# Kernel optimization log

Hardware: AMD Instinct MI355X
Metric: run time of the kernel (lower is better)

## Reference

```python
import jax, jax.numpy as jnp
import numpy as np

VOCAB, D, MAX_LEN = 32000, 256, 128
BATCH, SEQ = 32, 128


def setup_inputs() -> dict:
    key = jax.random.key(0)
    ks = jax.random.split(key, 8)
    s = 1.0 / np.sqrt(D)  # torch nn.Linear default init scale
    X = jax.random.randint(ks[0], (BATCH, SEQ), 0, VOCAB)
    emb = jax.random.normal(ks[1], (VOCAB, D), dtype=jnp.float32)
    W_l = jax.random.uniform(ks[2], (D, D), minval=-s, maxval=s, dtype=jnp.float32)
    b_l = jax.random.uniform(ks[3], (D,), minval=-s, maxval=s, dtype=jnp.float32)
    W_r = jax.random.uniform(ks[4], (D, D), minval=-s, maxval=s, dtype=jnp.float32)
    b_r = jax.random.uniform(ks[5], (D,), minval=-s, maxval=s, dtype=jnp.float32)
    W_rn = jax.random.uniform(ks[6], (D, D), minval=-s, maxval=s, dtype=jnp.float32)
    b_rn = jax.random.uniform(ks[7], (D,), minval=-s, maxval=s, dtype=jnp.float32)
    return {"X": X, "emb": emb, "W_l": W_l, "b_l": b_l,
            "W_r": W_r, "b_r": b_r, "W_rn": W_rn, "b_rn": b_rn}


def reference(X, emb, W_l, b_l, W_r, b_r, W_rn, b_rn):
    X = X[:, :MAX_LEN]
    n = X.shape[1]
    Xe = emb[X]                               # (B, n, D) embedding lookup
    Xl = Xe @ W_l.T + b_l                     # (B, n, D)
    Xr = Xe @ W_r.T + b_r                     # (B, n, D)
    # pairwise: pair[b, i, j] = relu(Xl[b, j] + Xr[b, i])  -> (B, n, n, D)
    pair = jax.nn.relu(Xl[:, None, :, :] + Xr[:, :, None, :])
    # linear_rn then sum over (i, j); by linearity: sum(pair) @ W_rn.T + n^2 * b_rn
    pooled = pair.sum(axis=(1, 2))            # (B, D)
    return pooled @ W_rn.T + (n * n) * b_rn   # (B, D)
```

## Files before the change

kernel.cpp:

```cpp
#include <hip/hip_runtime.h>

#define D 256
#define S 128
#define B 32
#define RT 8
#define DC 16

__device__ __forceinline__ float dot4(float4 a, float4 b) {
    return a.x * b.x + a.y * b.y + a.z * b.z + a.w * b.w;
}

__global__ __launch_bounds__(256) void k1_gemm(
    const int* __restrict__ X, const float* __restrict__ emb,
    const float* __restrict__ Wl, const float* __restrict__ bl,
    const float* __restrict__ Wr, const float* __restrict__ br,
    float* __restrict__ Xl, float* __restrict__ Xr)
{
    __shared__ float4 As[RT][D / 4];

    const int tid = threadIdx.x;
    const int rowBase = blockIdx.x * RT;

    {
        const int f0 = tid;
        const int f1 = tid + 256;
        const int r0 = f0 >> 6, kf0 = f0 & 63;
        const int r1 = f1 >> 6, kf1 = f1 & 63;
        const int tok0 = X[rowBase + r0];
        const int tok1 = X[rowBase + r1];
        As[r0][kf0] = ((const float4*)(emb + (size_t)tok0 * D))[kf0];
        As[r1][kf1] = ((const float4*)(emb + (size_t)tok1 * D))[kf1];
    }
    __syncthreads();

    const int d = tid;
    const float4* __restrict__ wl4 = (const float4*)(Wl + (size_t)d * D);
    const float4* __restrict__ wr4 = (const float4*)(Wr + (size_t)d * D);

    float accl[RT], accr[RT];
#pragma unroll
    for (int r = 0; r < RT; ++r) { accl[r] = 0.f; accr[r] = 0.f; }

#pragma unroll 4
    for (int kk = 0; kk < D / 4; ++kk) {
        const float4 wlv = wl4[kk];
        const float4 wrv = wr4[kk];
#pragma unroll
        for (int r = 0; r < RT; ++r) {
            const float4 a = As[r][kk];
            accl[r] += dot4(a, wlv);
            accr[r] += dot4(a, wrv);
        }
    }
    const float bld = bl[d], brd = br[d];
#pragma unroll
    for (int r = 0; r < RT; ++r) {
        Xl[(size_t)(rowBase + r) * D + d] = accl[r] + bld;
        Xr[(size_t)(rowBase + r) * D + d] = accr[r] + brd;
    }
}

__global__ __launch_bounds__(256) void k2_pairsum(
    const float* __restrict__ Xl, const float* __restrict__ Xr,
    float* __restrict__ pooled)
{
    __shared__ float lxl[S * DC];
    __shared__ float lxr[S * DC];
    __shared__ float red[256];

    const int b   = blockIdx.x >> 4;
    const int dc  = blockIdx.x & 15;
    const int tid = threadIdx.x;
    const int dl  = tid & (DC - 1);
    const int ig  = tid >> 4;

    const size_t base = (size_t)b * S * D + (size_t)dc * DC;
    {
        float4* lxl4 = (float4*)lxl;
        float4* lxr4 = (float4*)lxr;
#pragma unroll
        for (int t = 0; t < 2; ++t) {
            const int e4 = tid + t * 256;
            const int j = e4 >> 2, df = e4 & 3;
            const float4* pl = (const float4*)(Xl + base + (size_t)j * D);
            const float4* pr = (const float4*)(Xr + base + (size_t)j * D);
            lxl4[e4] = pl[df];
            lxr4[e4] = pr[df];
        }
    }
    __syncthreads();

    float xr[8];
    float sr = 0.f;
#pragma unroll
    for (int u = 0; u < 8; ++u) {
        xr[u] = lxr[(ig * 8 + u) * DC + dl];
        sr += xr[u];
    }

    float sabs = 0.f, sxl = 0.f;
#pragma unroll 4
    for (int j = 0; j < S; ++j) {
        const float x = lxl[j * DC + dl];
        sxl += x;
#pragma unroll
        for (int u = 0; u < 8; ++u)
            sabs += fabsf(x + xr[u]);
    }

    red[tid] = sabs + (float)S * sr;
    __syncthreads();

    if (tid < DC) {
        float tot = 0.f;
#pragma unroll
        for (int g = 0; g < 16; ++g) tot += red[g * DC + tid];
        pooled[(size_t)b * D + (size_t)dc * DC + tid] =
            0.5f * ((float)S * sxl + tot);
    }
}

__global__ __launch_bounds__(256) void k3_out(
    const float* __restrict__ pooled, const float* __restrict__ Wrn,
    const float* __restrict__ brn, float* __restrict__ out)
{
    __shared__ float lp[D];
    __shared__ float red[256];
    const int bb = blockIdx.x >> 3;
    const int dc = blockIdx.x & 7;
    const int tid = threadIdx.x;
    lp[tid] = pooled[(size_t)bb * D + tid];
    __syncthreads();

    const int dl = tid & 31;
    const int kg = tid >> 5;
    const int d = dc * 32 + dl;
    const float4* __restrict__ w4 = (const float4*)(Wrn + (size_t)d * D) + kg * 8;
    const float4* __restrict__ p4 = (const float4*)lp + kg * 8;
    float acc = 0.f;
#pragma unroll
    for (int f = 0; f < 8; ++f) acc += dot4(w4[f], p4[f]);

    red[tid] = acc;
    __syncthreads();
    if (tid < 32) {
        float s = 0.f;
#pragma unroll
        for (int g = 0; g < 8; ++g) s += red[g * 32 + tid];
        out[(size_t)bb * D + dc * 32 + tid] = s + (float)(S * S) * brn[dc * 32 + tid];
    }
}

extern "C" void kernel_launch(void* const* d_in, const int* in_sizes, int n_in,
                              void* d_out, int out_size, void* d_ws, size_t ws_size,
                              hipStream_t stream) {
    const int*   X   = (const int*)d_in[0];
    const float* emb = (const float*)d_in[1];
    const float* Wl  = (const float*)d_in[2];
    const float* bl  = (const float*)d_in[3];
    const float* Wr  = (const float*)d_in[4];
    const float* br  = (const float*)d_in[5];
    const float* Wrn = (const float*)d_in[6];
    const float* brn = (const float*)d_in[7];
    float* out = (float*)d_out;

    float* ws     = (float*)d_ws;
    float* Xl     = ws;
    float* Xr     = ws + (size_t)B * S * D;
    float* pooled = ws + 2 * (size_t)B * S * D;

    k1_gemm<<<(B * S) / RT, 256, 0, stream>>>(X, emb, Wl, bl, Wr, br, Xl, Xr);
    k2_pairsum<<<B * (D / DC), 256, 0, stream>>>(Xl, Xr, pooled);
    k3_out<<<B * 8, 256, 0, stream>>>(pooled, Wrn, brn, out);
}
```

Measured before the change: 135.6 us.

## Compute embedding projections with bf16 MFMA instead of fp32 FMA loops

Adds a kernel that casts W_l and W_r to bf16 in workspace, and replaces the scalar fp32 projection GEMM with a 16x16x32 bf16 MFMA kernel. Each block converts 16 gathered embedding rows to bf16 in shared memory and computes one of the two projections. The aim is to move the dominant GEMM cost onto matrix cores. In exchange it adds an extra kernel launch and lowers input precision to bf16, which may perturb the pairwise relu sums.

```diff
diff --git a/kernel.cpp b/kernel.cpp
--- a/kernel.cpp
+++ b/kernel.cpp
@@ -3,60 +3,99 @@
 #define D 256
 #define S 128
 #define B 32
-#define RT 8
 #define DC 16
+
+typedef __attribute__((ext_vector_type(8))) short bf16x8;
+typedef __attribute__((ext_vector_type(4))) float f32x4;
+
+__device__ __forceinline__ unsigned short f2bf(float f) {
+    union { float f; unsigned u; } v; v.f = f;
+    unsigned r = v.u + 0x7FFFu + ((v.u >> 16) & 1u);
+    return (unsigned short)(r >> 16);
+}
 
 __device__ __forceinline__ float dot4(float4 a, float4 b) {
     return a.x * b.x + a.y * b.y + a.z * b.z + a.w * b.w;
 }
 
-__global__ __launch_bounds__(256) void k1_gemm(
+__global__ __launch_bounds__(256) void k0_cast(
+    const float* __restrict__ Wl, const float* __restrict__ Wr,
+    unsigned short* __restrict__ Wb)
+{
+    const int idx = blockIdx.x * 256 + threadIdx.x;
+    const int e = idx * 4;
+    const int n = e >> 8, k = e & 255;
+    const float* src = (n < 256) ? (Wl + (size_t)n * D + k)
+                                 : (Wr + (size_t)(n - 256) * D + k);
+    const float4 f = *(const float4*)src;
+    ushort4 h;
+    h.x = f2bf(f.x); h.y = f2bf(f.y); h.z = f2bf(f.z); h.w = f2bf(f.w);
+    *(ushort4*)(Wb + (size_t)n * D + k) = h;
+}
+
+__global__ __launch_bounds__(256) void k1_mfma(
     const int* __restrict__ X, const float* __restrict__ emb,
-    const float* __restrict__ Wl, const float* __restrict__ bl,
-    const float* __restrict__ Wr, const float* __restrict__ br,
+    const unsigned short* __restrict__ Wb,
+    const float* __restrict__ bl, const float* __restrict__ br,
     float* __restrict__ Xl, float* __restrict__ Xr)
 {
-    __shared__ float4 As[RT][D / 4];
+    constexpr int LDA = 264;
+    __shared__ unsigned short Asb[16 * LDA];
 
     const int tid = threadIdx.x;
-    const int rowBase = blockIdx.x * RT;
+    const int rowBase = (blockIdx.x >> 1) * 16;
+    const int half = blockIdx.x & 1;
 
     {
-        const int f0 = tid;
-        const int f1 = tid + 256;
-        const int r0 = f0 >> 6, kf0 = f0 & 63;
-        const int r1 = f1 >> 6, kf1 = f1 & 63;
-        const int tok0 = X[rowBase + r0];
-        const int tok1 = X[rowBase + r1];
-        As[r0][kf0] = ((const float4*)(emb + (size_t)tok0 * D))[kf0];
-        As[r1][kf1] = ((const float4*)(emb + (size_t)tok1 * D))[kf1];
-    }
-    __syncthreads();
-
-    const int d = tid;
-    const float4* __restrict__ wl4 = (const float4*)(Wl + (size_t)d * D);
-    const float4* __restrict__ wr4 = (const float4*)(Wr + (size_t)d * D);
-
-    float accl[RT], accr[RT];
-#pragma unroll
-    for (int r = 0; r < RT; ++r) { accl[r] = 0.f; accr[r] = 0.f; }
-
-#pragma unroll 4
-    for (int kk = 0; kk < D / 4; ++kk) {
-        const float4 wlv = wl4[kk];
-        const float4 wrv = wr4[kk];
-#pragma unroll
-        for (int r = 0; r < RT; ++r) {
-            const float4 a = As[r][kk];
-            accl[r] += dot4(a, wlv);
-            accr[r] += dot4(a, wrv);
-        }
-    }
-    const float bld = bl[d], brd = br[d];
-#pragma unroll
-    for (int r = 0; r < RT; ++r) {
-        Xl[(size_t)(rowBase + r) * D + d] = accl[r] + bld;
-        Xr[(size_t)(rowBase + r) * D + d] = accr[r] + brd;
+        const int r = tid >> 4;
+        const int c0 = (tid & 15) * 16;
+        const int tok = X[rowBase + r];
+        const float* src = emb + (size_t)tok * D + c0;
+        unsigned short* dst = Asb + r * LDA + c0;
+#pragma unroll
+        for (int j4 = 0; j4 < 4; ++j4) {
+            const float4 f = ((const float4*)src)[j4];
+            ushort4 h;
+            h.x = f2bf(f.x); h.y = f2bf(f.y); h.z = f2bf(f.z); h.w = f2bf(f.w);
+            ((ushort4*)dst)[j4] = h;
+        }
+    }
+    __syncthreads();
+
+    const int w  = tid >> 6;
+    const int l  = tid & 63;
+    const int lm = l & 15;
+    const int lq = l >> 4;
+
+    const unsigned short* aptr = Asb + lm * LDA + lq * 8;
+    const int n_base = half * 256 + w * 64;
+    const unsigned short* bptr = Wb + (size_t)(n_base + lm) * D + lq * 8;
+
+    f32x4 acc[4];
+#pragma unroll
+    for (int t = 0; t < 4; ++t) acc[t] = (f32x4){0.f, 0.f, 0.f, 0.f};
+
+#pragma unroll
+    for (int ks = 0; ks < 8; ++ks) {
+        const bf16x8 a = *(const bf16x8*)(aptr + ks * 32);
+#pragma unroll
+        for (int t = 0; t < 4; ++t) {
+            const bf16x8 b = *(const bf16x8*)(bptr + (size_t)t * 16 * D + ks * 32);
+            acc[t] = __builtin_amdgcn_mfma_f32_16x16x32_bf16(a, b, acc[t], 0, 0, 0);
+        }
+    }
+
+    const float* __restrict__ bias = half ? br : bl;
+    float* __restrict__ Obase = half ? Xr : Xl;
+#pragma unroll
+    for (int t = 0; t < 4; ++t) {
+        const int col = w * 64 + t * 16 + lm;
+        const float bv = bias[col];
+#pragma unroll
+        for (int i = 0; i < 4; ++i) {
+            const int row = rowBase + lq * 4 + i;
+            Obase[(size_t)row * D + col] = acc[t][i] + bv;
+        }
     }
 }
 
@@ -168,8 +207,10 @@
     float* Xl     = ws;
     float* Xr     = ws + (size_t)B * S * D;
     float* pooled = ws + 2 * (size_t)B * S * D;
-
-    k1_gemm<<<(B * S) / RT, 256, 0, stream>>>(X, emb, Wl, bl, Wr, br, Xl, Xr);
+    unsigned short* Wb = (unsigned short*)(pooled + B * D);
+
+    k0_cast<<<128, 256, 0, stream>>>(Wl, Wr, Wb);
+    k1_mfma<<<512, 256, 0, stream>>>(X, emb, Wb, bl, br, Xl, Xr);
     k2_pairsum<<<B * (D / DC), 256, 0, stream>>>(Xl, Xr, pooled);
     k3_out<<<B * 8, 256, 0, stream>>>(pooled, Wrn, brn, out);
 }
```

After: 112.7 us. 1.2x faster.
